# Optimization experiments

Hardware: AMD Instinct MI355X
Metric: run time of the kernel (lower is better)

Reference implementation:

```python
import jax, jax.numpy as jnp
import numpy as np

B, N, F, H, MH = 8, 1024, 768, 12, 3072
DH = F // H
EPS = 1e-5

def _ln(x, g, b):
    mu = jnp.mean(x, axis=-1, keepdims=True)
    var = jnp.mean(jnp.square(x - mu), axis=-1, keepdims=True)
    return (x - mu) * jax.lax.rsqrt(var + EPS) * g + b

def setup_inputs() -> dict:
    key = jax.random.key(0)
    ks = jax.random.split(key, 16)
    s = 1.0 / np.sqrt(F)
    sm = 1.0 / np.sqrt(MH)
    return {
        "x": jax.random.normal(ks[0], (B, N, F), dtype=jnp.float32),
        "Wq": jax.random.uniform(ks[1], (F, F), jnp.float32, -s, s),
        "bq": jax.random.uniform(ks[2], (F,), jnp.float32, -s, s),
        "Wk": jax.random.uniform(ks[3], (F, F), jnp.float32, -s, s),
        "bk": jax.random.uniform(ks[4], (F,), jnp.float32, -s, s),
        "Wv": jax.random.uniform(ks[5], (F, F), jnp.float32, -s, s),
        "bv": jax.random.uniform(ks[6], (F,), jnp.float32, -s, s),
        "Wo": jax.random.uniform(ks[7], (F, F), jnp.float32, -s, s),
        "bo": jax.random.uniform(ks[8], (F,), jnp.float32, -s, s),
        "ln1_g": jnp.ones((F,), jnp.float32),
        "ln1_b": jnp.zeros((F,), jnp.float32),
        "ln2_g": jnp.ones((F,), jnp.float32),
        "ln2_b": jnp.zeros((F,), jnp.float32),
        "W1": jax.random.uniform(ks[9], (F, MH), jnp.float32, -s, s),
        "b1": jax.random.uniform(ks[10], (MH,), jnp.float32, -s, s),
        "W2": jax.random.uniform(ks[11], (MH, F), jnp.float32, -sm, sm),
        "b2": jax.random.uniform(ks[12], (F,), jnp.float32, -sm, sm),
    }

def reference(x, Wq, bq, Wk, bk, Wv, bv, Wo, bo, ln1_g, ln1_b, ln2_g, ln2_b, W1, b1, W2, b2):
    xn = _ln(x, ln1_g, ln1_b)
    # low-rank (here full-rank, rank=-1) QKV projections, split into heads -> [b,h,n,dh]
    q = (xn @ Wq + bq).reshape(B, N, H, DH).transpose(0, 2, 1, 3)
    k = (xn @ Wk + bk).reshape(B, N, H, DH).transpose(0, 2, 1, 3)
    v = (xn @ Wv + bv).reshape(B, N, H, DH).transpose(0, 2, 1, 3)
    # note: original scales by sqrt(feats), NOT sqrt(d_head)
    score = jax.nn.softmax(jnp.einsum('bhif,bhjf->bhij', q, k) / jnp.sqrt(jnp.float32(F)), axis=-1)
    attn = jnp.einsum('bhij,bhjf->bhif', score, v)
    attn = attn.transpose(0, 2, 1, 3).reshape(B, N, F)
    out = (attn @ Wo + bo) + x  # dropout p=0.0
    h = _ln(out, ln2_g, ln2_b)
    h = jax.nn.gelu(h @ W1 + b1, approximate=False)
    h = jax.nn.gelu(h @ W2 + b2, approximate=False)  # second GELU per source
    return h + out
```

## Files before the change

### kernel.cpp

```cpp
#include <hip/hip_runtime.h>
#include <math.h>

#define B_ 8
#define N_ 1024
#define F_ 768
#define H_ 12
#define DH_ 64
#define MH_ 3072
#define MROWS (B_ * N_)

typedef unsigned short u16;
typedef unsigned int u32;
typedef __bf16 bf16x8 __attribute__((ext_vector_type(8)));
typedef float f32x4 __attribute__((ext_vector_type(4)));

__device__ inline f32x4 mfma16(bf16x8 a, bf16x8 b, f32x4 c) {
  return __builtin_amdgcn_mfma_f32_16x16x32_bf16(a, b, c, 0, 0, 0);
}

__device__ inline u16 f2bu(float f) {
  u32 b = __builtin_bit_cast(u32, f);
  b += 0x7fffu + ((b >> 16) & 1u);
  return (u16)(b >> 16);
}
__device__ inline float bu2f(u16 u) {
  u32 x = ((u32)u) << 16;
  return __builtin_bit_cast(float, x);
}
__device__ inline float gelu_exact(float x) {
  return 0.5f * x * (1.0f + erff(x * 0.70710678118654752f));
}

#define AS1 __attribute__((address_space(1)))
#define AS3 __attribute__((address_space(3)))
__device__ inline void glds16(const void* g, void* l) {
  __builtin_amdgcn_global_load_lds((const AS1 void*)g, (AS3 void*)l, 16, 0, 0);
}

__global__ __launch_bounds__(256) void prep_weights(
    const float* __restrict__ Wq, const float* __restrict__ Wk,
    const float* __restrict__ Wv, const float* __restrict__ Wo,
    const float* __restrict__ W1, const float* __restrict__ W2,
    u16* __restrict__ Wqkvt, u16* __restrict__ Wot,
    u16* __restrict__ W1t, u16* __restrict__ W2t) {
  __shared__ float tile[64][65];
  int z = blockIdx.z;
  const float* in; u16* out; int R, C;
  if (z == 0)      { in = Wq; out = Wqkvt;                       R = 768;  C = 768; }
  else if (z == 1) { in = Wk; out = Wqkvt + 768 * 768;           R = 768;  C = 768; }
  else if (z == 2) { in = Wv; out = Wqkvt + 2 * 768 * 768;       R = 768;  C = 768; }
  else if (z == 3) { in = Wo; out = Wot;                         R = 768;  C = 768; }
  else if (z == 4) { in = W1; out = W1t;                         R = 768;  C = 3072; }
  else             { in = W2; out = W2t;                         R = 3072; C = 768; }
  int r0 = blockIdx.y << 6, c0 = blockIdx.x << 6;
  if (r0 >= R || c0 >= C) return;
  int t = threadIdx.x;
#pragma unroll
  for (int i = 0; i < 16; ++i) {
    int idx = t + (i << 8);
    int r = idx >> 6, c = idx & 63;
    tile[r][c] = in[(size_t)(r0 + r) * C + (c0 + c)];
  }
  __syncthreads();
#pragma unroll
  for (int i = 0; i < 16; ++i) {
    int idx = t + (i << 8);
    int rr = idx >> 6, cc = idx & 63;
    out[(size_t)(c0 + rr) * R + (r0 + cc)] = f2bu(tile[cc][rr]);
  }
}

__global__ __launch_bounds__(256) void transpose_v(
    const u16* __restrict__ in, u16* __restrict__ out, int R, int C) {
  __shared__ float tile[64][65];
  size_t base = (size_t)blockIdx.z * (size_t)R * (size_t)C;
  int r0 = blockIdx.y << 6, c0 = blockIdx.x << 6;
  int t = threadIdx.x;
#pragma unroll
  for (int i = 0; i < 16; ++i) {
    int idx = t + (i << 8);
    int r = idx >> 6, c = idx & 63;
    tile[r][c] = bu2f(in[base + (size_t)(r0 + r) * C + (c0 + c)]);
  }
  __syncthreads();
#pragma unroll
  for (int i = 0; i < 16; ++i) {
    int idx = t + (i << 8);
    int rr = idx >> 6, cc = idx & 63;
    out[base + (size_t)(c0 + rr) * R + (r0 + cc)] = f2bu(tile[cc][rr]);
  }
}

__global__ __launch_bounds__(256) void ln_to_bf16(
    const float* __restrict__ X, const float* __restrict__ gw,
    const float* __restrict__ bw, u16* __restrict__ Y) {
  int row = blockIdx.x;
  int t = threadIdx.x;
  const float* xr = X + (size_t)row * F_;
  float v0 = xr[t], v1 = xr[t + 256], v2 = xr[t + 512];
  float s = v0 + v1 + v2;
  float ss = v0 * v0 + v1 * v1 + v2 * v2;
#pragma unroll
  for (int off = 1; off < 64; off <<= 1) {
    s += __shfl_xor(s, off, 64);
    ss += __shfl_xor(ss, off, 64);
  }
  __shared__ float red[8];
  int wid = t >> 6, lane = t & 63;
  if (lane == 0) { red[wid] = s; red[4 + wid] = ss; }
  __syncthreads();
  s = red[0] + red[1] + red[2] + red[3];
  ss = red[4] + red[5] + red[6] + red[7];
  float mu = s * (1.0f / F_);
  float var = ss * (1.0f / F_) - mu * mu;
  float rstd = rsqrtf(var + 1e-5f);
  u16* yr = Y + (size_t)row * F_;
  yr[t] = f2bu((v0 - mu) * rstd * gw[t] + bw[t]);
  yr[t + 256] = f2bu((v1 - mu) * rstd * gw[t + 256] + bw[t + 256]);
  yr[t + 512] = f2bu((v2 - mu) * rstd * gw[t + 512] + bw[t + 512]);
}

template <int MODE>
__global__ __launch_bounds__(256, 4) void gemm_t(
    const u16* __restrict__ A, const u16* __restrict__ Bt,
    const float* __restrict__ b0, const float* __restrict__ b1,
    const float* __restrict__ b2, void* __restrict__ outp,
    const float* __restrict__ resid, int Ndim, int Kdim, float qscale) {
  __shared__ __attribute__((aligned(16))) u16 As[2][128][32];
  __shared__ __attribute__((aligned(16))) u16 Bs[2][64][32];
  int t = threadIdx.x;
  int lane = t & 63, wid = t >> 6;

  int nwg = gridDim.x;
  int q8 = nwg >> 3;
  int bid = blockIdx.x;
  int swz = (bid & 7) * q8 + (bid >> 3);
  int nnt = Ndim >> 6;
  int mt = swz / nnt, nt = swz - mt * nnt;
  int row0 = mt << 7, col0 = nt << 6;

  int wr = (wid >> 1) << 6;
  int wc = (wid & 1) << 5;
  int lr = lane & 15, lk = (lane >> 4) << 3;
  int rbase = (lane >> 4) << 2;
  f32x4 zero = {0.f, 0.f, 0.f, 0.f};
  f32x4 acc[4][2];
#pragma unroll
  for (int m = 0; m < 4; ++m)
#pragma unroll
    for (int n = 0; n < 2; ++n) acc[m][n] = zero;

  int srow = (wid << 4) + (lane >> 2);
  int scol = (lane & 3) << 3;
  const u16* Ag = A + (size_t)(row0 + srow) * Kdim + scol;
  const u16* Bg = Bt + (size_t)(col0 + srow) * Kdim + scol;
  char* AsB = (char*)&As[0][0][0] + (wid << 10);
  char* BsB = (char*)&Bs[0][0][0] + (wid << 10);
  size_t half = (size_t)64 * Kdim;

  auto STAGE = [&](int buf, int kt) {
    glds16(Ag + kt, AsB + (buf << 13));
    glds16(Ag + kt + half, AsB + (buf << 13) + 4096);
    glds16(Bg + kt, BsB + (buf << 12));
  };

  STAGE(0, 0);
  __syncthreads();
  int nk = Kdim >> 5;
  for (int ki = 0; ki < nk; ++ki) {
    int buf = ki & 1;
    if (ki + 1 < nk) STAGE(buf ^ 1, (ki + 1) << 5);
    bf16x8 af[4], bfr[2];
#pragma unroll
    for (int m = 0; m < 4; ++m) af[m] = *(const bf16x8*)&As[buf][wr + (m << 4) + lr][lk];
#pragma unroll
    for (int n = 0; n < 2; ++n) bfr[n] = *(const bf16x8*)&Bs[buf][wc + (n << 4) + lr][lk];
#pragma unroll
    for (int m = 0; m < 4; ++m)
#pragma unroll
      for (int n = 0; n < 2; ++n) acc[m][n] = mfma16(af[m], bfr[n], acc[m][n]);
    __syncthreads();
  }

#pragma unroll
  for (int n = 0; n < 2; ++n) {
    int col = col0 + wc + (n << 4) + lr;
    float bc;
    int sub = 0, hh = 0, dh = 0;
    float sc = 1.0f;
    if constexpr (MODE == 0) {
      sub = (col >= 1536) ? 2 : (col >= 768 ? 1 : 0);
      int c = col - sub * 768;
      bc = (sub == 0) ? b0[c] : (sub == 1 ? b1[c] : b2[c]);
      hh = c >> 6; dh = c & 63;
      sc = (sub == 0) ? qscale : 1.0f;
    } else {
      bc = b0[col];
    }
#pragma unroll
    for (int m = 0; m < 4; ++m) {
#pragma unroll
      for (int r = 0; r < 4; ++r) {
        int row = row0 + wr + (m << 4) + rbase + r;
        float val = acc[m][n][r] + bc;
        if constexpr (MODE == 0) {
          int bb = row >> 10, nn = row & 1023;
          ((u16*)outp)[(size_t)sub * 6291456 +
                       ((((size_t)bb * H_ + hh) << 10) + nn) * DH_ + dh] = f2bu(val * sc);
        } else if constexpr (MODE == 1) {
          val += resid[(size_t)row * Ndim + col];
          ((float*)outp)[(size_t)row * Ndim + col] = val;
        } else if constexpr (MODE == 2) {
          ((u16*)outp)[(size_t)row * Ndim + col] = f2bu(gelu_exact(val));
        } else {
          val = gelu_exact(val) + resid[(size_t)row * Ndim + col];
          ((float*)outp)[(size_t)row * Ndim + col] = val;
        }
      }
    }
  }
}

__global__ __launch_bounds__(256, 3) void attn_fwd(
    const u16* __restrict__ Q, const u16* __restrict__ K,
    const u16* __restrict__ Vt, u16* __restrict__ Aout) {
  __shared__ __attribute__((aligned(16))) u16 Ks[64][72];
  __shared__ __attribute__((aligned(16))) u16 Vs[64][72];
  __shared__ __attribute__((aligned(16))) u16 Ps[4][32][72];
  int t = threadIdx.x, lane = t & 63, wid = t >> 6;

  int bid = blockIdx.x;
  int swz = (bid & 7) * 96 + (bid >> 3);
  int bh = swz >> 3;
  int qt = swz & 7;
  int q0 = (qt << 7) + (wid << 5);

  int lr = lane & 15, lk = (lane >> 4) << 3;
  int rbase = (lane >> 4) << 2;

  bf16x8 qf[2][2];
#pragma unroll
  for (int m = 0; m < 2; ++m)
#pragma unroll
    for (int ks = 0; ks < 2; ++ks)
      qf[m][ks] = *(const bf16x8*)&Q[((size_t)bh * N_ + q0 + (m << 4) + lr) * DH_ + (ks << 5) + lk];

  float lsum[2][4];
  f32x4 zero = {0.f, 0.f, 0.f, 0.f};
  f32x4 Oacc[2][4];
#pragma unroll
  for (int m = 0; m < 2; ++m) {
#pragma unroll
    for (int r = 0; r < 4; ++r) lsum[m][r] = 0.f;
#pragma unroll
    for (int nd = 0; nd < 4; ++nd) Oacc[m][nd] = zero;
  }

  int srow = t >> 3;
  int scol = (t & 7) << 3;
  const u16* Kg = K + ((size_t)bh * N_ + srow) * DH_ + scol;
  const u16* Vg = Vt + ((size_t)bh * DH_ + srow) * N_ + scol;

  uint4 kr0, kr1, vr0, vr1;
  auto LOADKV = [&](int kt) {
    kr0 = *(const uint4*)(Kg + (size_t)(kt << 6) * DH_);
    kr1 = *(const uint4*)(Kg + (size_t)((kt << 6) + 32) * DH_);
    vr0 = *(const uint4*)(Vg + (kt << 6));
    vr1 = *(const uint4*)(Vg + (size_t)32 * N_ + (kt << 6));
  };
  LOADKV(0);

  for (int kt = 0; kt < 16; ++kt) {
    __syncthreads();
    *(uint4*)&Ks[srow][scol]      = kr0;
    *(uint4*)&Ks[srow + 32][scol] = kr1;
    *(uint4*)&Vs[srow][scol]      = vr0;
    *(uint4*)&Vs[srow + 32][scol] = vr1;
    if (kt + 1 < 16) LOADKV(kt + 1);
    __syncthreads();

    f32x4 s[2][4];
#pragma unroll
    for (int m = 0; m < 2; ++m)
#pragma unroll
      for (int n = 0; n < 4; ++n) s[m][n] = zero;
#pragma unroll
    for (int ks = 0; ks < 2; ++ks) {
      bf16x8 kf[4];
#pragma unroll
      for (int n = 0; n < 4; ++n) kf[n] = *(const bf16x8*)&Ks[(n << 4) + lr][(ks << 5) + lk];
#pragma unroll
      for (int m = 0; m < 2; ++m)
#pragma unroll
        for (int n = 0; n < 4; ++n) s[m][n] = mfma16(qf[m][ks], kf[n], s[m][n]);
    }

#pragma unroll
    for (int m = 0; m < 2; ++m)
#pragma unroll
      for (int n = 0; n < 4; ++n)
#pragma unroll
        for (int r = 0; r < 4; ++r) {
          float p = exp2f(s[m][n][r]);
          lsum[m][r] += p;
          Ps[wid][(m << 4) + rbase + r][(n << 4) + lr] = f2bu(p);
        }

#pragma unroll
    for (int ks = 0; ks < 2; ++ks) {
      bf16x8 pf[2], vf[4];
#pragma unroll
      for (int m = 0; m < 2; ++m) pf[m] = *(const bf16x8*)&Ps[wid][(m << 4) + lr][(ks << 5) + lk];
#pragma unroll
      for (int nd = 0; nd < 4; ++nd) vf[nd] = *(const bf16x8*)&Vs[(nd << 4) + lr][(ks << 5) + lk];
#pragma unroll
      for (int m = 0; m < 2; ++m)
#pragma unroll
        for (int nd = 0; nd < 4; ++nd) Oacc[m][nd] = mfma16(pf[m], vf[nd], Oacc[m][nd]);
    }
  }

  int b = bh / H_, h = bh % H_;
#pragma unroll
  for (int m = 0; m < 2; ++m)
#pragma unroll
    for (int r = 0; r < 4; ++r) {
      float sv = lsum[m][r];
#pragma unroll
      for (int off = 1; off < 16; off <<= 1) sv += __shfl_xor(sv, off, 64);
      float inv = 1.0f / sv;
      int row = q0 + (m << 4) + rbase + r;
      size_t orow = ((size_t)b * N_ + row) * F_ + (size_t)h * DH_;
#pragma unroll
      for (int nd = 0; nd < 4; ++nd)
        Aout[orow + (nd << 4) + lr] = f2bu(Oacc[m][nd][r] * inv);
    }
}

extern "C" void kernel_launch(void* const* d_in, const int* in_sizes, int n_in,
                              void* d_out, int out_size, void* d_ws, size_t ws_size,
                              hipStream_t stream) {
  (void)in_sizes; (void)n_in; (void)out_size; (void)ws_size;
  const float* x   = (const float*)d_in[0];
  const float* Wq  = (const float*)d_in[1];
  const float* bq  = (const float*)d_in[2];
  const float* Wk  = (const float*)d_in[3];
  const float* bk  = (const float*)d_in[4];
  const float* Wv  = (const float*)d_in[5];
  const float* bv  = (const float*)d_in[6];
  const float* Wo  = (const float*)d_in[7];
  const float* bo  = (const float*)d_in[8];
  const float* g1  = (const float*)d_in[9];
  const float* bn1 = (const float*)d_in[10];
  const float* g2  = (const float*)d_in[11];
  const float* bn2 = (const float*)d_in[12];
  const float* W1  = (const float*)d_in[13];
  const float* b1  = (const float*)d_in[14];
  const float* W2  = (const float*)d_in[15];
  const float* b2  = (const float*)d_in[16];

  char* ws = (char*)d_ws;
  size_t off = 0;
  auto alloc = [&](size_t bytes) {
    char* p = ws + off;
    off += (bytes + 255) & ~(size_t)255;
    return p;
  };
  u16* Wqkvt = (u16*)alloc((size_t)3 * F_ * F_ * 2);
  u16* Wot  = (u16*)alloc((size_t)F_ * F_ * 2);
  u16* W1t  = (u16*)alloc((size_t)MH_ * F_ * 2);
  u16* W2t  = (u16*)alloc((size_t)MH_ * F_ * 2);
  u16* xn  = (u16*)alloc((size_t)MROWS * F_ * 2);
  u16* qb  = (u16*)alloc((size_t)B_ * H_ * N_ * DH_ * 2);
  u16* kb  = (u16*)alloc((size_t)B_ * H_ * N_ * DH_ * 2);
  u16* vb  = (u16*)alloc((size_t)B_ * H_ * N_ * DH_ * 2);
  u16* vt  = (u16*)alloc((size_t)B_ * H_ * N_ * DH_ * 2);
  u16* attn = (u16*)alloc((size_t)MROWS * F_ * 2);
  float* outb = (float*)alloc((size_t)MROWS * F_ * 4);
  u16* h1 = qb;
  u16* hn = xn;

  const float QSCALE = 0.052058773227f;

  dim3 blk(256);
  prep_weights<<<dim3(48, 48, 6), blk, 0, stream>>>(Wq, Wk, Wv, Wo, W1, W2,
                                                    Wqkvt, Wot, W1t, W2t);
  ln_to_bf16<<<dim3(MROWS), blk, 0, stream>>>(x, g1, bn1, xn);
  gemm_t<0><<<dim3(64 * 36), blk, 0, stream>>>(xn, Wqkvt, bq, bk, bv, qb,
                                               nullptr, 3 * F_, F_, QSCALE);
  transpose_v<<<dim3(1, 16, 96), blk, 0, stream>>>(vb, vt, N_, DH_);
  attn_fwd<<<dim3(768), blk, 0, stream>>>(qb, kb, vt, attn);
  gemm_t<1><<<dim3(64 * 12), blk, 0, stream>>>(attn, Wot, bo, nullptr, nullptr,
                                               outb, x, F_, F_, 1.0f);
  ln_to_bf16<<<dim3(MROWS), blk, 0, stream>>>(outb, g2, bn2, hn);
  gemm_t<2><<<dim3(64 * 48), blk, 0, stream>>>(hn, W1t, b1, nullptr, nullptr,
                                               h1, nullptr, MH_, F_, 1.0f);
  gemm_t<3><<<dim3(64 * 12), blk, 0, stream>>>(h1, W2t, b2, nullptr, nullptr,
                                               d_out, outb, F_, MH_, 1.0f);
}
```

Before: 317.7 us.

## Widen GEMM tiles to 128x128 with a four-stage LDS pipeline

The GEMM kernel now uses 128x128 output tiles, so each wave computes a 64x64 sub-tile with 16 accumulators. The LDS double buffer becomes a 4-slot ring: loads are issued three k-steps ahead and gated by explicit vmcnt waits plus one barrier per iteration. MFMA sections run at raised wave priority. This is meant to raise data reuse per LDS load and hide global-load latency, at the cost of more registers, lower occupancy (launch bounds 2), and half as many workgroups, which can leave CUs idle on the smaller GEMMs.

```diff
diff --git a/kernel.cpp b/kernel.cpp
--- a/kernel.cpp
+++ b/kernel.cpp
@@ -121,13 +121,13 @@
 }
 
 template <int MODE>
-__global__ __launch_bounds__(256, 4) void gemm_t(
+__global__ __launch_bounds__(256, 2) void gemm_t(
     const u16* __restrict__ A, const u16* __restrict__ Bt,
     const float* __restrict__ b0, const float* __restrict__ b1,
     const float* __restrict__ b2, void* __restrict__ outp,
     const float* __restrict__ resid, int Ndim, int Kdim, float qscale) {
-  __shared__ __attribute__((aligned(16))) u16 As[2][128][32];
-  __shared__ __attribute__((aligned(16))) u16 Bs[2][64][32];
+  __shared__ __attribute__((aligned(16))) u16 As4[4][128][32];
+  __shared__ __attribute__((aligned(16))) u16 Bs4[4][128][32];
   int t = threadIdx.x;
   int lane = t & 63, wid = t >> 6;
 
@@ -135,55 +135,65 @@
   int q8 = nwg >> 3;
   int bid = blockIdx.x;
   int swz = (bid & 7) * q8 + (bid >> 3);
-  int nnt = Ndim >> 6;
+  int nnt = Ndim >> 7;
   int mt = swz / nnt, nt = swz - mt * nnt;
-  int row0 = mt << 7, col0 = nt << 6;
-
-  int wr = (wid >> 1) << 6;
-  int wc = (wid & 1) << 5;
+  int row0 = mt << 7, col0 = nt << 7;
+
+  int wr = (wid >> 1) << 6, wc = (wid & 1) << 6;
   int lr = lane & 15, lk = (lane >> 4) << 3;
   int rbase = (lane >> 4) << 2;
   f32x4 zero = {0.f, 0.f, 0.f, 0.f};
-  f32x4 acc[4][2];
+  f32x4 acc[4][4];
 #pragma unroll
   for (int m = 0; m < 4; ++m)
 #pragma unroll
-    for (int n = 0; n < 2; ++n) acc[m][n] = zero;
-
-  int srow = (wid << 4) + (lane >> 2);
-  int scol = (lane & 3) << 3;
+    for (int n = 0; n < 4; ++n) acc[m][n] = zero;
+
+  int o0 = (wid << 10) + (lane << 4);
+  int srow = o0 >> 6;
+  int scol = (o0 & 63) >> 1;
   const u16* Ag = A + (size_t)(row0 + srow) * Kdim + scol;
   const u16* Bg = Bt + (size_t)(col0 + srow) * Kdim + scol;
-  char* AsB = (char*)&As[0][0][0] + (wid << 10);
-  char* BsB = (char*)&Bs[0][0][0] + (wid << 10);
+  char* AsB = (char*)&As4[0][0][0] + (wid << 10);
+  char* BsB = (char*)&Bs4[0][0][0] + (wid << 10);
   size_t half = (size_t)64 * Kdim;
 
-  auto STAGE = [&](int buf, int kt) {
-    glds16(Ag + kt, AsB + (buf << 13));
-    glds16(Ag + kt + half, AsB + (buf << 13) + 4096);
-    glds16(Bg + kt, BsB + (buf << 12));
+  int nk = Kdim >> 5;
+  auto STAGE = [&](int i) {
+    if (i >= nk) return;
+    int so = (i & 3) << 13;
+    int kt = i << 5;
+    glds16(Ag + kt, AsB + so);
+    glds16(Ag + kt + half, AsB + so + 4096);
+    glds16(Bg + kt, BsB + so);
+    glds16(Bg + kt + half, BsB + so + 4096);
   };
 
-  STAGE(0, 0);
-  __syncthreads();
-  int nk = Kdim >> 5;
+  STAGE(0); STAGE(1); STAGE(2);
+
   for (int ki = 0; ki < nk; ++ki) {
-    int buf = ki & 1;
-    if (ki + 1 < nk) STAGE(buf ^ 1, (ki + 1) << 5);
-    bf16x8 af[4], bfr[2];
-#pragma unroll
-    for (int m = 0; m < 4; ++m) af[m] = *(const bf16x8*)&As[buf][wr + (m << 4) + lr][lk];
-#pragma unroll
-    for (int n = 0; n < 2; ++n) bfr[n] = *(const bf16x8*)&Bs[buf][wc + (n << 4) + lr][lk];
+    if (ki < nk - 2)       asm volatile("s_waitcnt vmcnt(8)" ::: "memory");
+    else if (ki == nk - 2) asm volatile("s_waitcnt vmcnt(4)" ::: "memory");
+    else                   asm volatile("s_waitcnt vmcnt(0)" ::: "memory");
+    __builtin_amdgcn_s_barrier();
+    __builtin_amdgcn_sched_barrier(0);
+    STAGE(ki + 3);
+    int sl = ki & 3;
+    bf16x8 af[4], bfr[4];
+#pragma unroll
+    for (int m = 0; m < 4; ++m) af[m] = *(const bf16x8*)&As4[sl][wr + (m << 4) + lr][lk];
+#pragma unroll
+    for (int n = 0; n < 4; ++n) bfr[n] = *(const bf16x8*)&Bs4[sl][wc + (n << 4) + lr][lk];
+    __builtin_amdgcn_s_setprio(1);
 #pragma unroll
     for (int m = 0; m < 4; ++m)
 #pragma unroll
-      for (int n = 0; n < 2; ++n) acc[m][n] = mfma16(af[m], bfr[n], acc[m][n]);
-    __syncthreads();
-  }
-
-#pragma unroll
-  for (int n = 0; n < 2; ++n) {
+      for (int n = 0; n < 4; ++n) acc[m][n] = mfma16(af[m], bfr[n], acc[m][n]);
+    __builtin_amdgcn_s_setprio(0);
+  }
+
+#pragma unroll
+  for (int n = 0; n < 4; ++n) {
     int col = col0 + wc + (n << 4) + lr;
     float bc;
     int sub = 0, hh = 0, dh = 0;
@@ -386,15 +396,15 @@
   prep_weights<<<dim3(48, 48, 6), blk, 0, stream>>>(Wq, Wk, Wv, Wo, W1, W2,
                                                     Wqkvt, Wot, W1t, W2t);
   ln_to_bf16<<<dim3(MROWS), blk, 0, stream>>>(x, g1, bn1, xn);
-  gemm_t<0><<<dim3(64 * 36), blk, 0, stream>>>(xn, Wqkvt, bq, bk, bv, qb,
+  gemm_t<0><<<dim3(64 * 18), blk, 0, stream>>>(xn, Wqkvt, bq, bk, bv, qb,
                                                nullptr, 3 * F_, F_, QSCALE);
   transpose_v<<<dim3(1, 16, 96), blk, 0, stream>>>(vb, vt, N_, DH_);
   attn_fwd<<<dim3(768), blk, 0, stream>>>(qb, kb, vt, attn);
-  gemm_t<1><<<dim3(64 * 12), blk, 0, stream>>>(attn, Wot, bo, nullptr, nullptr,
-                                               outb, x, F_, F_, 1.0f);
+  gemm_t<1><<<dim3(64 * 6), blk, 0, stream>>>(attn, Wot, bo, nullptr, nullptr,
+                                              outb, x, F_, F_, 1.0f);
   ln_to_bf16<<<dim3(MROWS), blk, 0, stream>>>(outb, g2, bn2, hn);
-  gemm_t<2><<<dim3(64 * 48), blk, 0, stream>>>(hn, W1t, b1, nullptr, nullptr,
+  gemm_t<2><<<dim3(64 * 24), blk, 0, stream>>>(hn, W1t, b1, nullptr, nullptr,
                                                h1, nullptr, MH_, F_, 1.0f);
-  gemm_t<3><<<dim3(64 * 12), blk, 0, stream>>>(h1, W2t, b2, nullptr, nullptr,
-                                               d_out, outb, F_, MH_, 1.0f);
-}
+  gemm_t<3><<<dim3(64 * 6), blk, 0, stream>>>(h1, W2t, b2, nullptr, nullptr,
+                                              d_out, outb, F_, MH_, 1.0f);
+}
```

Result: slower. 325.7 us (+2.5%).

## Use 128x128 GEMM tiles with 32x32x16 MFMA and XOR-swizzled LDS

Applied to the files above, without the earlier changes.

The shared GEMM kernel moves from 128x64 tiles built from 16x16x32 MFMAs to 128x128 tiles built from 32x32x16 MFMAs, so each wave computes a 64x64 sub-tile. LDS columns are XOR-swizzled on both the global-to-LDS staging and the fragment reads to cut bank conflicts. The aim is more reuse per loaded byte and fewer instructions per FLOP. In exchange it uses more LDS and accumulator registers, lowers the occupancy hint to 3, and halves the grid, so the N=768 GEMMs launch only 384 workgroups.

```diff
diff --git a/kernel.cpp b/kernel.cpp
--- a/kernel.cpp
+++ b/kernel.cpp
@@ -13,9 +13,13 @@
 typedef unsigned int u32;
 typedef __bf16 bf16x8 __attribute__((ext_vector_type(8)));
 typedef float f32x4 __attribute__((ext_vector_type(4)));
+typedef float f32x16 __attribute__((ext_vector_type(16)));
 
 __device__ inline f32x4 mfma16(bf16x8 a, bf16x8 b, f32x4 c) {
   return __builtin_amdgcn_mfma_f32_16x16x32_bf16(a, b, c, 0, 0, 0);
+}
+__device__ inline f32x16 mfma32(bf16x8 a, bf16x8 b, f32x16 c) {
+  return __builtin_amdgcn_mfma_f32_32x32x16_bf16(a, b, c, 0, 0, 0);
 }
 
 __device__ inline u16 f2bu(float f) {
@@ -121,13 +125,13 @@
 }
 
 template <int MODE>
-__global__ __launch_bounds__(256, 4) void gemm_t(
+__global__ __launch_bounds__(256, 3) void gemm_t(
     const u16* __restrict__ A, const u16* __restrict__ Bt,
     const float* __restrict__ b0, const float* __restrict__ b1,
     const float* __restrict__ b2, void* __restrict__ outp,
     const float* __restrict__ resid, int Ndim, int Kdim, float qscale) {
   __shared__ __attribute__((aligned(16))) u16 As[2][128][32];
-  __shared__ __attribute__((aligned(16))) u16 Bs[2][64][32];
+  __shared__ __attribute__((aligned(16))) u16 Bs[2][128][32];
   int t = threadIdx.x;
   int lane = t & 63, wid = t >> 6;
 
@@ -135,23 +139,21 @@
   int q8 = nwg >> 3;
   int bid = blockIdx.x;
   int swz = (bid & 7) * q8 + (bid >> 3);
-  int nnt = Ndim >> 6;
+  int nnt = Ndim >> 7;
   int mt = swz / nnt, nt = swz - mt * nnt;
-  int row0 = mt << 7, col0 = nt << 6;
-
-  int wr = (wid >> 1) << 6;
-  int wc = (wid & 1) << 5;
-  int lr = lane & 15, lk = (lane >> 4) << 3;
-  int rbase = (lane >> 4) << 2;
-  f32x4 zero = {0.f, 0.f, 0.f, 0.f};
-  f32x4 acc[4][2];
-#pragma unroll
-  for (int m = 0; m < 4; ++m)
-#pragma unroll
-    for (int n = 0; n < 2; ++n) acc[m][n] = zero;
+  int row0 = mt << 7, col0 = nt << 7;
+
+  int wr = (wid >> 1) << 6, wc = (wid & 1) << 6;
+  int l31 = lane & 31, kg = lane >> 5;
+  int qx = lane & 3;
+  f32x16 acc[2][2];
+#pragma unroll
+  for (int m = 0; m < 2; ++m)
+#pragma unroll
+    for (int n = 0; n < 2; ++n) acc[m][n] = (f32x16)(0.f);
 
   int srow = (wid << 4) + (lane >> 2);
-  int scol = (lane & 3) << 3;
+  int scol = (((lane & 3) ^ ((lane >> 2) & 3)) << 3);
   const u16* Ag = A + (size_t)(row0 + srow) * Kdim + scol;
   const u16* Bg = Bt + (size_t)(col0 + srow) * Kdim + scol;
   char* AsB = (char*)&As[0][0][0] + (wid << 10);
@@ -159,10 +161,15 @@
   size_t half = (size_t)64 * Kdim;
 
   auto STAGE = [&](int buf, int kt) {
-    glds16(Ag + kt, AsB + (buf << 13));
-    glds16(Ag + kt + half, AsB + (buf << 13) + 4096);
-    glds16(Bg + kt, BsB + (buf << 12));
+    int bo = buf << 13;
+    glds16(Ag + kt, AsB + bo);
+    glds16(Ag + kt + half, AsB + bo + 4096);
+    glds16(Bg + kt, BsB + bo);
+    glds16(Bg + kt + half, BsB + bo + 4096);
   };
+
+  int cq0 = (kg ^ qx) << 3;
+  int cq1 = ((2 | kg) ^ qx) << 3;
 
   STAGE(0, 0);
   __syncthreads();
@@ -170,21 +177,31 @@
   for (int ki = 0; ki < nk; ++ki) {
     int buf = ki & 1;
     if (ki + 1 < nk) STAGE(buf ^ 1, (ki + 1) << 5);
-    bf16x8 af[4], bfr[2];
-#pragma unroll
-    for (int m = 0; m < 4; ++m) af[m] = *(const bf16x8*)&As[buf][wr + (m << 4) + lr][lk];
-#pragma unroll
-    for (int n = 0; n < 2; ++n) bfr[n] = *(const bf16x8*)&Bs[buf][wc + (n << 4) + lr][lk];
-#pragma unroll
-    for (int m = 0; m < 4; ++m)
-#pragma unroll
-      for (int n = 0; n < 2; ++n) acc[m][n] = mfma16(af[m], bfr[n], acc[m][n]);
+    bf16x8 af[2][2], bfr[2][2];
+#pragma unroll
+    for (int m = 0; m < 2; ++m) {
+      af[m][0] = *(const bf16x8*)&As[buf][wr + (m << 5) + l31][cq0];
+      af[m][1] = *(const bf16x8*)&As[buf][wr + (m << 5) + l31][cq1];
+    }
+#pragma unroll
+    for (int n = 0; n < 2; ++n) {
+      bfr[n][0] = *(const bf16x8*)&Bs[buf][wc + (n << 5) + l31][cq0];
+      bfr[n][1] = *(const bf16x8*)&Bs[buf][wc + (n << 5) + l31][cq1];
+    }
+#pragma unroll
+    for (int ks = 0; ks < 2; ++ks)
+#pragma unroll
+      for (int m = 0; m < 2; ++m)
+#pragma unroll
+        for (int n = 0; n < 2; ++n)
+          acc[m][n] = mfma32(af[m][ks], bfr[n][ks], acc[m][n]);
     __syncthreads();
   }
 
+  int rext = kg << 2;
 #pragma unroll
   for (int n = 0; n < 2; ++n) {
-    int col = col0 + wc + (n << 4) + lr;
+    int col = col0 + wc + (n << 5) + l31;
     float bc;
     int sub = 0, hh = 0, dh = 0;
     float sc = 1.0f;
@@ -198,10 +215,10 @@
       bc = b0[col];
     }
 #pragma unroll
-    for (int m = 0; m < 4; ++m) {
-#pragma unroll
-      for (int r = 0; r < 4; ++r) {
-        int row = row0 + wr + (m << 4) + rbase + r;
+    for (int m = 0; m < 2; ++m) {
+#pragma unroll
+      for (int r = 0; r < 16; ++r) {
+        int row = row0 + wr + (m << 5) + (r & 3) + ((r >> 2) << 3) + rext;
         float val = acc[m][n][r] + bc;
         if constexpr (MODE == 0) {
           int bb = row >> 10, nn = row & 1023;
@@ -386,15 +403,15 @@
   prep_weights<<<dim3(48, 48, 6), blk, 0, stream>>>(Wq, Wk, Wv, Wo, W1, W2,
                                                     Wqkvt, Wot, W1t, W2t);
   ln_to_bf16<<<dim3(MROWS), blk, 0, stream>>>(x, g1, bn1, xn);
-  gemm_t<0><<<dim3(64 * 36), blk, 0, stream>>>(xn, Wqkvt, bq, bk, bv, qb,
+  gemm_t<0><<<dim3(64 * 18), blk, 0, stream>>>(xn, Wqkvt, bq, bk, bv, qb,
                                                nullptr, 3 * F_, F_, QSCALE);
   transpose_v<<<dim3(1, 16, 96), blk, 0, stream>>>(vb, vt, N_, DH_);
   attn_fwd<<<dim3(768), blk, 0, stream>>>(qb, kb, vt, attn);
-  gemm_t<1><<<dim3(64 * 12), blk, 0, stream>>>(attn, Wot, bo, nullptr, nullptr,
-                                               outb, x, F_, F_, 1.0f);
+  gemm_t<1><<<dim3(64 * 6), blk, 0, stream>>>(attn, Wot, bo, nullptr, nullptr,
+                                              outb, x, F_, F_, 1.0f);
   ln_to_bf16<<<dim3(MROWS), blk, 0, stream>>>(outb, g2, bn2, hn);
-  gemm_t<2><<<dim3(64 * 48), blk, 0, stream>>>(hn, W1t, b1, nullptr, nullptr,
+  gemm_t<2><<<dim3(64 * 24), blk, 0, stream>>>(hn, W1t, b1, nullptr, nullptr,
                                                h1, nullptr, MH_, F_, 1.0f);
-  gemm_t<3><<<dim3(64 * 12), blk, 0, stream>>>(h1, W2t, b2, nullptr, nullptr,
-                                               d_out, outb, F_, MH_, 1.0f);
-}
+  gemm_t<3><<<dim3(64 * 6), blk, 0, stream>>>(h1, W2t, b2, nullptr, nullptr,
+                                              d_out, outb, F_, MH_, 1.0f);
+}
```

New measurement: 317.2 us. Within noise of the previous version (-0.2%).
